# Performance work log

Measured on AMD Instinct MI355X. Metric: run time of the kernel, lower is better.

The kernel has to match this reference:

```python
import jax, jax.numpy as jnp
import numpy as np

D = 768  # feature_dim


def setup_inputs() -> dict:
    key = jax.random.key(0)
    ks = jax.random.split(key, 8)
    B, L = 8, 2048
    vision_features = jax.random.normal(ks[0], (B, L, D), dtype=jnp.float32)
    language_features = jax.random.normal(ks[1], (B, L, D), dtype=jnp.float32)
    s = 1.0 / np.sqrt(D)
    Wv = jax.random.uniform(ks[2], (D, D), jnp.float32, -s, s)
    bv = jax.random.uniform(ks[3], (D,), jnp.float32, -s, s)
    Wl = jax.random.uniform(ks[4], (D, D), jnp.float32, -s, s)
    bl = jax.random.uniform(ks[5], (D,), jnp.float32, -s, s)
    so = 1.0 / np.sqrt(2 * D)
    Wo = jax.random.uniform(ks[6], (D, 2 * D), jnp.float32, -so, so)
    bo = jax.random.uniform(ks[7], (D,), jnp.float32, -so, so)
    return {
        "vision_features": vision_features,
        "language_features": language_features,
        "Wv": Wv, "bv": bv, "Wl": Wl, "bl": bl, "Wo": Wo, "bo": bo,
    }


def reference(vision_features, language_features, Wv, bv, Wl, bl, Wo, bo):
    # linear projections (torch Linear: x @ W^T + b)
    vp = jnp.einsum('bld,ed->ble', vision_features, Wv) + bv      # [B,L,D]
    lp = jnp.einsum('bld,ed->ble', language_features, Wl) + bl    # [B,L,D]
    # unscaled bidirectional attention
    sim = jnp.einsum('bid,bjd->bij', vp, lp)                      # [B,L,L]
    attn = jax.nn.softmax(sim, axis=-1)
    aligned_vision = jnp.einsum('bij,bjd->bid', attn, vp)         # [B,L,D]
    aligned_language = jnp.einsum('bij,bid->bjd', attn, lp)       # attn^T @ lp -> [B,L,D]
    combined = jnp.concatenate([aligned_vision, aligned_language], axis=-1)  # [B,L,2D]
    return jnp.einsum('blc,ec->ble', combined, Wo) + bo           # [B,L,D]
```

## Files before the change

### kernel.cpp

```cpp
#include <hip/hip_runtime.h>
#include <stdint.h>

typedef __attribute__((ext_vector_type(8))) short bf16x8;
typedef __attribute__((ext_vector_type(4))) float f32x4;

__device__ __forceinline__ float b2f(short h) {
  return __uint_as_float(((unsigned)(unsigned short)h) << 16);
}
__device__ __forceinline__ short f2b(float f) {
  unsigned u = __float_as_uint(f);
  u += 0x7fffu + ((u >> 16) & 1u);
  return (short)(u >> 16);
}

__device__ __forceinline__ int swz(int r) { return (r & 6) << 2; }

__device__ __forceinline__ void glds16(const void* g, void* l) {
  __builtin_amdgcn_global_load_lds(
      (const __attribute__((address_space(1))) void*)g,
      (__attribute__((address_space(3))) void*)l, 16, 0, 0);
}

__device__ __forceinline__ void xcd_decode(int C, int RSX, int RPZ,
                                           int& z, int& rowB, int& colB) {
  int id = blockIdx.x;
  int xcd = id & 7, slot = id >> 3;
  int rs = xcd * RSX + slot / C;
  colB = (slot % C) * 128;
  z = rs / RPZ;
  rowB = (rs % RPZ) * 128;
}

__global__ __launch_bounds__(256) void cvt_kernel(
    const float* __restrict__ S0, short* __restrict__ H0, short* __restrict__ L0,
    const float* __restrict__ S1, short* __restrict__ H1, short* __restrict__ L1,
    const float* __restrict__ S2, short* __restrict__ H2, short* __restrict__ L2,
    int n0, int n1, int n2) {
  int g = blockIdx.x * 256 + threadIdx.x;
  const float* s;
  short* h;
  short* l;
  if (g < n0) {
    s = S0 + (size_t)g * 8;
    h = H0 + (size_t)g * 8;
    l = L0 + (size_t)g * 8;
  } else if (g < n0 + n1) {
    size_t t = (size_t)(g - n0);
    s = S1 + t * 8;
    h = H1 + t * 8;
    l = L1 + t * 8;
  } else {
    size_t t = (size_t)(g - n0 - n1);
    s = S2 + t * 8;
    h = H2 + t * 8;
    l = L2 + t * 8;
  }
  float4 v0 = *reinterpret_cast<const float4*>(s);
  float4 v1 = *reinterpret_cast<const float4*>(s + 4);
  float vv[8] = {v0.x, v0.y, v0.z, v0.w, v1.x, v1.y, v1.z, v1.w};
  bf16x8 th, tl;
#pragma unroll
  for (int j = 0; j < 8; ++j) {
    short hh = f2b(vv[j]);
    th[j] = hh;
    tl[j] = f2b(vv[j] - b2f(hh));
  }
  *reinterpret_cast<bf16x8*>(h) = th;
  *reinterpret_cast<bf16x8*>(l) = tl;
}

__global__ __launch_bounds__(256) void rowsum_kernel(const short* __restrict__ P,
                                                     float* __restrict__ invL) {
  int wave = threadIdx.x >> 6, lane = threadIdx.x & 63;
  size_t row = (size_t)blockIdx.x * 4 + wave;
  const short* p = P + row * 2048;
  float s = 0.f;
#pragma unroll
  for (int it = 0; it < 4; ++it) {
    bf16x8 x = *reinterpret_cast<const bf16x8*>(&p[it * 512 + lane * 8]);
#pragma unroll
    for (int j = 0; j < 8; ++j) s += b2f(x[j]);
  }
#pragma unroll
  for (int m = 32; m; m >>= 1) s += __shfl_xor(s, m);
  if (lane == 0) invL[row] = 1.0f / s;
}

__global__ __launch_bounds__(256) void scale_transpose_kernel(
    const short* __restrict__ lp, const float* __restrict__ invL,
    short* __restrict__ lpsT) {
  __shared__ alignas(16) short T[64 * 64];
  int id = blockIdx.x;
  int z = id / 384, r = id % 384;
  int it = r / 12, dt = r % 12;
  int i0 = it * 64, d0 = dt * 64;
  const short* src = lp + (size_t)z * 2048 * 768;
  const float* Lz = invL + (size_t)z * 2048;
  int t = threadIdx.x;
#pragma unroll
  for (int q = 0; q < 2; ++q) {
    int v = t * 2 + q;
    int ii = v >> 3, dc = (v & 7) * 8;
    float s = Lz[i0 + ii];
    bf16x8 x = *reinterpret_cast<const bf16x8*>(&src[(size_t)(i0 + ii) * 768 + d0 + dc]);
    bf16x8 y;
#pragma unroll
    for (int j = 0; j < 8; ++j) y[j] = f2b(b2f(x[j]) * s);
    *reinterpret_cast<bf16x8*>(&T[ii * 64 + (dc ^ ((ii & 7) << 3))]) = y;
  }
  __syncthreads();
  short* dst = lpsT + (size_t)z * 768 * 2048;
#pragma unroll
  for (int q = 0; q < 2; ++q) {
    int v = t * 2 + q;
    int dd = v >> 3, is = (v & 7) * 8;
    bf16x8 y;
#pragma unroll
    for (int s2 = 0; s2 < 8; ++s2) {
      int rr = is + s2;
      y[s2] = T[rr * 64 + (dd ^ ((rr & 7) << 3))];
    }
    *reinterpret_cast<bf16x8*>(&dst[(size_t)(d0 + dd) * 2048 + i0 + is]) = y;
  }
}

__global__ __launch_bounds__(256) void transpose_inplace_kernel(short* __restrict__ P) {
  __shared__ alignas(16) short Ta[64 * 64];
  __shared__ alignas(16) short Tb[64 * 64];
  int id = blockIdx.x;
  int z = id >> 10, r = id & 1023;
  int a = r >> 5, b = r & 31;
  if (a > b) return;
  short* Pz = P + (size_t)z * 2048 * 2048;
  int t = threadIdx.x;
#pragma unroll
  for (int q = 0; q < 2; ++q) {
    int v = t * 2 + q;
    int ii = v >> 3, cc = (v & 7) * 8;
    bf16x8 x = *reinterpret_cast<const bf16x8*>(&Pz[(size_t)(a * 64 + ii) * 2048 + b * 64 + cc]);
    *reinterpret_cast<bf16x8*>(&Ta[ii * 64 + (cc ^ ((ii & 7) << 3))]) = x;
    if (a != b) {
      bf16x8 y = *reinterpret_cast<const bf16x8*>(&Pz[(size_t)(b * 64 + ii) * 2048 + a * 64 + cc]);
      *reinterpret_cast<bf16x8*>(&Tb[ii * 64 + (cc ^ ((ii & 7) << 3))]) = y;
    }
  }
  __syncthreads();
#pragma unroll
  for (int q = 0; q < 2; ++q) {
    int v = t * 2 + q;
    int rr = v >> 3, cs = (v & 7) * 8;
    bf16x8 x, y;
#pragma unroll
    for (int s2 = 0; s2 < 8; ++s2) {
      int rs = cs + s2;
      x[s2] = Ta[rs * 64 + (rr ^ ((rs & 7) << 3))];
      if (a != b) y[s2] = Tb[rs * 64 + (rr ^ ((rs & 7) << 3))];
    }
    *reinterpret_cast<bf16x8*>(&Pz[(size_t)(b * 64 + rr) * 2048 + a * 64 + cs]) = x;
    if (a != b)
      *reinterpret_cast<bf16x8*>(&Pz[(size_t)(a * 64 + rr) * 2048 + b * 64 + cs]) = y;
  }
}

template <bool LO>
__global__ __launch_bounds__(256) void projg_kernel(
    const short* __restrict__ Ah, const short* __restrict__ Al,
    const short* __restrict__ Bh, const short* __restrict__ Bl,
    const float* __restrict__ bias,
    short* __restrict__ Ch, short* __restrict__ Cl) {
  __shared__ alignas(16) short AsH[128 * 32];
  __shared__ alignas(16) short AsL[128 * 32];
  __shared__ alignas(16) short BsH[128 * 32];
  __shared__ alignas(16) short BsL[128 * 32];
  const int tid = threadIdx.x;
  int z, rowBase, colBase;
  xcd_decode(6, 16, 128, z, rowBase, colBase);
  (void)z;
  const int lane = tid & 63;
  const int ln = lane & 15;
  const int qd = lane >> 4;
  const int w = tid >> 6;
  const int wr = w >> 1, wc = w & 1;

  f32x4 acc[4][4];
#pragma unroll
  for (int i = 0; i < 4; ++i)
#pragma unroll
    for (int j = 0; j < 4; ++j) acc[i][j] = 0.f;

  for (int kb = 0; kb < 768; kb += 32) {
#pragma unroll
    for (int q = 0; q < 2; ++q) {
      int c = q * 256 + tid;
      int r = c >> 2;
      int k0 = ((c & 3) << 3) ^ swz(r);
      size_t ao = (size_t)(rowBase + r) * 768 + kb + k0;
      size_t bo = (size_t)(colBase + r) * 768 + kb + k0;
      glds16(&Ah[ao], &AsH[c * 8]);
      glds16(&Al[ao], &AsL[c * 8]);
      glds16(&Bh[bo], &BsH[c * 8]);
      glds16(&Bl[bo], &BsL[c * 8]);
    }
    __syncthreads();
    bf16x8 ah[4], bh[4], t[4];
#pragma unroll
    for (int rt = 0; rt < 4; ++rt) {
      int m = wr * 64 + rt * 16 + ln;
      ah[rt] = *reinterpret_cast<const bf16x8*>(&AsH[m * 32 + ((qd * 8) ^ swz(m))]);
    }
#pragma unroll
    for (int ct = 0; ct < 4; ++ct) {
      int n = wc * 64 + ct * 16 + ln;
      bh[ct] = *reinterpret_cast<const bf16x8*>(&BsH[n * 32 + ((qd * 8) ^ swz(n))]);
    }
#pragma unroll
    for (int rt = 0; rt < 4; ++rt)
#pragma unroll
      for (int ct = 0; ct < 4; ++ct)
        acc[rt][ct] = __builtin_amdgcn_mfma_f32_16x16x32_bf16(ah[rt], bh[ct], acc[rt][ct], 0, 0, 0);
#pragma unroll
    for (int rt = 0; rt < 4; ++rt) {
      int m = wr * 64 + rt * 16 + ln;
      t[rt] = *reinterpret_cast<const bf16x8*>(&AsL[m * 32 + ((qd * 8) ^ swz(m))]);
    }
#pragma unroll
    for (int rt = 0; rt < 4; ++rt)
#pragma unroll
      for (int ct = 0; ct < 4; ++ct)
        acc[rt][ct] = __builtin_amdgcn_mfma_f32_16x16x32_bf16(t[rt], bh[ct], acc[rt][ct], 0, 0, 0);
#pragma unroll
    for (int ct = 0; ct < 4; ++ct) {
      int n = wc * 64 + ct * 16 + ln;
      t[ct] = *reinterpret_cast<const bf16x8*>(&BsL[n * 32 + ((qd * 8) ^ swz(n))]);
    }
#pragma unroll
    for (int rt = 0; rt < 4; ++rt)
#pragma unroll
      for (int ct = 0; ct < 4; ++ct)
        acc[rt][ct] = __builtin_amdgcn_mfma_f32_16x16x32_bf16(ah[rt], t[ct], acc[rt][ct], 0, 0, 0);
    __syncthreads();
  }

#pragma unroll
  for (int rt = 0; rt < 4; ++rt) {
    int row0 = rowBase + wr * 64 + rt * 16 + qd * 4;
#pragma unroll
    for (int ct = 0; ct < 4; ++ct) {
      int col = colBase + wc * 64 + ct * 16 + ln;
      float bb = bias[col];
      f32x4 a = acc[rt][ct];
#pragma unroll
      for (int r = 0; r < 4; ++r) {
        float val = a[r] + bb;
        short h = f2b(val);
        Ch[(size_t)(row0 + r) * 768 + col] = h;
        if constexpr (LO) Cl[(size_t)(row0 + r) * 768 + col] = f2b(val - b2f(h));
      }
    }
  }
}

__global__ __launch_bounds__(256) void sim2_kernel(const short* __restrict__ vp,
                                                   const short* __restrict__ lph,
                                                   const short* __restrict__ lpl,
                                                   short* __restrict__ P) {
  __shared__ alignas(16) short As[128 * 32];
  __shared__ alignas(16) short Bh[128 * 32];
  __shared__ alignas(16) short Bl[128 * 32];
  const int tid = threadIdx.x;
  int z, rowBase, colBase;
  xcd_decode(16, 16, 16, z, rowBase, colBase);
  const short* Az = vp + (size_t)z * 2048 * 768;
  const short* B0 = lph + (size_t)z * 2048 * 768;
  const short* B1 = lpl + (size_t)z * 2048 * 768;
  const int lane = tid & 63;
  const int ln = lane & 15;
  const int qd = lane >> 4;
  const int w = tid >> 6;
  const int wr = w >> 1, wc = w & 1;

  f32x4 acc[4][4];
#pragma unroll
  for (int i = 0; i < 4; ++i)
#pragma unroll
    for (int j = 0; j < 4; ++j) acc[i][j] = 0.f;

  for (int kb = 0; kb < 768; kb += 32) {
#pragma unroll
    for (int q = 0; q < 2; ++q) {
      int c = q * 256 + tid;
      int r = c >> 2;
      int k0 = ((c & 3) << 3) ^ swz(r);
      glds16(&Az[(size_t)(rowBase + r) * 768 + kb + k0], &As[c * 8]);
      glds16(&B0[(size_t)(colBase + r) * 768 + kb + k0], &Bh[c * 8]);
      glds16(&B1[(size_t)(colBase + r) * 768 + kb + k0], &Bl[c * 8]);
    }
    __syncthreads();
    bf16x8 af[4], bf[4];
#pragma unroll
    for (int rt = 0; rt < 4; ++rt) {
      int m = wr * 64 + rt * 16 + ln;
      af[rt] = *reinterpret_cast<const bf16x8*>(&As[m * 32 + ((qd * 8) ^ swz(m))]);
    }
#pragma unroll
    for (int ct = 0; ct < 4; ++ct) {
      int n = wc * 64 + ct * 16 + ln;
      bf[ct] = *reinterpret_cast<const bf16x8*>(&Bh[n * 32 + ((qd * 8) ^ swz(n))]);
    }
#pragma unroll
    for (int rt = 0; rt < 4; ++rt)
#pragma unroll
      for (int ct = 0; ct < 4; ++ct)
        acc[rt][ct] = __builtin_amdgcn_mfma_f32_16x16x32_bf16(af[rt], bf[ct], acc[rt][ct], 0, 0, 0);
#pragma unroll
    for (int ct = 0; ct < 4; ++ct) {
      int n = wc * 64 + ct * 16 + ln;
      bf[ct] = *reinterpret_cast<const bf16x8*>(&Bl[n * 32 + ((qd * 8) ^ swz(n))]);
    }
#pragma unroll
    for (int rt = 0; rt < 4; ++rt)
#pragma unroll
      for (int ct = 0; ct < 4; ++ct)
        acc[rt][ct] = __builtin_amdgcn_mfma_f32_16x16x32_bf16(af[rt], bf[ct], acc[rt][ct], 0, 0, 0);
    __syncthreads();
  }

  short* Pz = P + (size_t)z * 2048 * 2048;
#pragma unroll
  for (int rt = 0; rt < 4; ++rt) {
    int row0 = rowBase + wr * 64 + rt * 16 + qd * 4;
#pragma unroll
    for (int ct = 0; ct < 4; ++ct) {
      int col = colBase + wc * 64 + ct * 16 + ln;
      f32x4 a = acc[rt][ct];
#pragma unroll
      for (int r = 0; r < 4; ++r)
        Pz[(size_t)(row0 + r) * 2048 + col] = f2b(__expf(a[r] - 20.0f));
    }
  }
}

template <int MODE, bool TB, bool SB, bool DUALA>
__global__ __launch_bounds__(256) void gemm_k(const short* __restrict__ A,
                                              const short* __restrict__ A2,
                                              const void* __restrict__ B,
                                              void* __restrict__ C,
                                              const float* __restrict__ bias,
                                              const float* __restrict__ invL,
                                              int C_, int RSX_, int RPZ_,
                                              int K, int ldA, int ldB, int ldC,
                                              long sA, long sB, long sC, long sL) {
  __shared__ alignas(16) short As[128 * 32];
  __shared__ alignas(16) short Bs[128 * 32];
  const int tid = threadIdx.x;
  int z, rowBase, colBase;
  xcd_decode(C_, RSX_, RPZ_, z, rowBase, colBase);
  const short* Az = A + (size_t)z * sA;
  const float* Lz = invL ? (invL + (size_t)z * sL) : nullptr;
  const int lane = tid & 63;
  const int ln = lane & 15;
  const int qd = lane >> 4;
  const int w = tid >> 6;
  const int wr = w >> 1, wc = w & 1;

  f32x4 acc[4][4];
#pragma unroll
  for (int i = 0; i < 4; ++i)
#pragma unroll
    for (int j = 0; j < 4; ++j) acc[i][j] = 0.f;

  for (int kb = 0; kb < K; kb += 32) {
#pragma unroll
    for (int q = 0; q < 2; ++q) {
      int c = q * 256 + tid;
      int r = c >> 2;
      int k0 = ((c & 3) << 3) ^ swz(r);
      int kk = kb + k0;
      const short* src;
      if constexpr (DUALA) {
        src = (kk < 768) ? &Az[(size_t)(rowBase + r) * 768 + kk]
                         : &A2[(size_t)(rowBase + r) * 768 + kk - 768];
      } else {
        src = &Az[(size_t)(rowBase + r) * ldA + kk];
      }
      glds16(src, &As[c * 8]);
    }
    if constexpr (TB) {
      const short* Bz = (const short*)B + (size_t)z * sB;
#pragma unroll
      for (int q = 0; q < 2; ++q) {
        int task = q * 256 + tid;
        int n = task & 127;
        int kc = (task >> 7) << 3;
        bf16x8 t;
#pragma unroll
        for (int s = 0; s < 8; ++s) {
          short v = Bz[(size_t)(kb + kc + s) * ldB + colBase + n];
          if constexpr (SB) v = f2b(b2f(v) * Lz[kb + kc + s]);
          t[s] = v;
        }
        *reinterpret_cast<bf16x8*>(&Bs[n * 32 + (kc ^ swz(n))]) = t;
      }
    } else {
      const short* Bz = (const short*)B + (size_t)z * sB;
#pragma unroll
      for (int q = 0; q < 2; ++q) {
        int c = q * 256 + tid;
        int r = c >> 2;
        int k0 = ((c & 3) << 3) ^ swz(r);
        glds16(&Bz[(size_t)(colBase + r) * ldB + kb + k0], &Bs[c * 8]);
      }
    }
    __syncthreads();
    bf16x8 af[4], bfv[4];
#pragma unroll
    for (int rt = 0; rt < 4; ++rt) {
      int m = wr * 64 + rt * 16 + ln;
      af[rt] = *reinterpret_cast<const bf16x8*>(&As[m * 32 + ((qd * 8) ^ swz(m))]);
    }
#pragma unroll
    for (int ct = 0; ct < 4; ++ct) {
      int n = wc * 64 + ct * 16 + ln;
      bfv[ct] = *reinterpret_cast<const bf16x8*>(&Bs[n * 32 + ((qd * 8) ^ swz(n))]);
    }
#pragma unroll
    for (int rt = 0; rt < 4; ++rt)
#pragma unroll
      for (int ct = 0; ct < 4; ++ct)
        acc[rt][ct] =
            __builtin_amdgcn_mfma_f32_16x16x32_bf16(af[rt], bfv[ct], acc[rt][ct], 0, 0, 0);
    __syncthreads();
  }

#pragma unroll
  for (int rt = 0; rt < 4; ++rt) {
    int row0 = rowBase + wr * 64 + rt * 16 + qd * 4;
#pragma unroll
    for (int ct = 0; ct < 4; ++ct) {
      int col = colBase + wc * 64 + ct * 16 + ln;
      f32x4 a = acc[rt][ct];
      if constexpr (MODE == 2) {
        short* Co = (short*)C + (size_t)z * sC;
#pragma unroll
        for (int r = 0; r < 4; ++r)
          Co[(size_t)(row0 + r) * ldC + col] = f2b(a[r] * Lz[row0 + r]);
      } else if constexpr (MODE == 3) {
        short* Co = (short*)C + (size_t)z * sC;
#pragma unroll
        for (int r = 0; r < 4; ++r) Co[(size_t)(row0 + r) * ldC + col] = f2b(a[r]);
      } else {
        float* Co = (float*)C + (size_t)z * sC;
        float bb = bias[col];
#pragma unroll
        for (int r = 0; r < 4; ++r) Co[(size_t)(row0 + r) * ldC + col] = a[r] + bb;
      }
    }
  }
}

extern "C" void kernel_launch(void* const* d_in, const int* in_sizes, int n_in,
                              void* d_out, int out_size, void* d_ws, size_t ws_size,
                              hipStream_t stream) {
  const float* vf = (const float*)d_in[0];
  const float* lf = (const float*)d_in[1];
  const float* Wv = (const float*)d_in[2];
  const float* bv = (const float*)d_in[3];
  const float* Wl = (const float*)d_in[4];
  const float* bl = (const float*)d_in[5];
  const float* Wo = (const float*)d_in[6];
  const float* bo = (const float*)d_in[7];

  constexpr int Bz = 8, L = 2048, D = 768, M = Bz * L, D2 = 2 * D;
  constexpr size_t PLANE = (size_t)M * D;
  constexpr size_t WPLANE = (size_t)D * D;

  char* wp = (char*)d_ws;
  auto alloc = [&](size_t bytes) {
    char* p = wp;
    wp += (bytes + 255) & ~(size_t)255;
    return p;
  };
  short* vp_hi = (short*)alloc(PLANE * 2);
  short* P     = (short*)alloc((size_t)Bz * L * L * 2);
  float* invL  = (float*)alloc((size_t)M * 4);

  size_t need_direct = (size_t)(wp - (char*)d_ws) + 2 * PLANE * 2 + 512;
  bool direct = ws_size >= need_direct;

  short *lp_hi, *lp_lo;
  if (direct) {
    lp_hi = (short*)alloc(PLANE * 2);
    lp_lo = (short*)alloc(PLANE * 2);
  } else {
    lp_hi = (short*)d_out;
    lp_lo = lp_hi + PLANE;
  }
  short* lpsT = lp_lo;
  short* av   = lp_hi;
  short* al   = vp_hi;
  short* woh = P + 2 * PLANE;
  short* wol = woh + (size_t)D * D2;
  float* out_tmp = direct ? (float*)d_out : (float*)P;

  short* fh  = P;
  short* fl  = P + PLANE;
  short* wvh = P + 2 * PLANE;
  short* wvl = wvh + WPLANE;
  short* wlh = wvl + WPLANE;
  short* wll = wlh + WPLANE;

  constexpr int GF  = (int)(PLANE / 8);
  constexpr int GW  = (int)(WPLANE / 8);
  constexpr int GWO = (int)((size_t)D * D2 / 8);

  cvt_kernel<<<dim3((GF + 2 * GW) / 256), 256, 0, stream>>>(
      vf, fh, fl, Wv, wvh, wvl, Wl, wlh, wll, GF, GW, GW);

  projg_kernel<false><<<dim3(768), 256, 0, stream>>>(fh, fl, wvh, wvl, bv, vp_hi, nullptr);

  cvt_kernel<<<dim3(GF / 256), 256, 0, stream>>>(
      lf, fh, fl, nullptr, nullptr, nullptr, nullptr, nullptr, nullptr, GF, 0, 0);

  projg_kernel<true><<<dim3(768), 256, 0, stream>>>(fh, fl, wlh, wll, bl, lp_hi, lp_lo);

  sim2_kernel<<<dim3(2048), 256, 0, stream>>>(vp_hi, lp_hi, lp_lo, P);

  rowsum_kernel<<<dim3(M / 4), 256, 0, stream>>>(P, invL);

  scale_transpose_kernel<<<dim3(3072), 256, 0, stream>>>(lp_hi, invL, lpsT);

  gemm_k<2, true, false, false><<<dim3(768), 256, 0, stream>>>(
      P, nullptr, vp_hi, av, nullptr, invL, 6, 16, 16, L, L, D, D,
      (long)L * L, (long)L * D, (long)L * D, (long)L);

  transpose_inplace_kernel<<<dim3(8192), 256, 0, stream>>>(P);

  gemm_k<3, false, false, false><<<dim3(768), 256, 0, stream>>>(
      P, nullptr, lpsT, al, nullptr, nullptr, 6, 16, 16, L, L, L, D,
      (long)L * L, (long)D * L, (long)L * D, (long)L);

  cvt_kernel<<<dim3(GWO / 256), 256, 0, stream>>>(
      Wo, woh, wol, nullptr, nullptr, nullptr, nullptr, nullptr, nullptr, GWO, 0, 0);

  gemm_k<4, false, false, true><<<dim3(768), 256, 0, stream>>>(
      av, al, woh, out_tmp, bo, nullptr, 6, 16, 128, D2, D, D2, D, 0, 0, 0, 0);

  if (!direct)
    hipMemcpyAsync(d_out, out_tmp, (size_t)M * D * 4, hipMemcpyDeviceToDevice, stream);
}
```

Before: 657.9 us.

## Use fp16 single-pass MFMA for similarity and fuse row sums via atomics

Result: faster. 643.6 us (-2.2%).

```diff
diff --git a/kernel.cpp b/kernel.cpp
--- a/kernel.cpp
+++ b/kernel.cpp
@@ -2,6 +2,7 @@
 #include <stdint.h>
 
 typedef __attribute__((ext_vector_type(8))) short bf16x8;
+typedef __attribute__((ext_vector_type(8))) _Float16 f16x8;
 typedef __attribute__((ext_vector_type(4))) float f32x4;
 
 __device__ __forceinline__ float b2f(short h) {
@@ -11,6 +12,13 @@
   unsigned u = __float_as_uint(f);
   u += 0x7fffu + ((u >> 16) & 1u);
   return (short)(u >> 16);
+}
+__device__ __forceinline__ short f2h(float f) {
+  _Float16 h = (_Float16)f;
+  return __builtin_bit_cast(short, h);
+}
+__device__ __forceinline__ float h2f(short s) {
+  return (float)__builtin_bit_cast(_Float16, s);
 }
 
 __device__ __forceinline__ int swz(int r) { return (r & 6) << 2; }
@@ -69,21 +77,14 @@
   *reinterpret_cast<bf16x8*>(l) = tl;
 }
 
-__global__ __launch_bounds__(256) void rowsum_kernel(const short* __restrict__ P,
-                                                     float* __restrict__ invL) {
-  int wave = threadIdx.x >> 6, lane = threadIdx.x & 63;
-  size_t row = (size_t)blockIdx.x * 4 + wave;
-  const short* p = P + row * 2048;
-  float s = 0.f;
-#pragma unroll
-  for (int it = 0; it < 4; ++it) {
-    bf16x8 x = *reinterpret_cast<const bf16x8*>(&p[it * 512 + lane * 8]);
-#pragma unroll
-    for (int j = 0; j < 8; ++j) s += b2f(x[j]);
-  }
-#pragma unroll
-  for (int m = 32; m; m >>= 1) s += __shfl_xor(s, m);
-  if (lane == 0) invL[row] = 1.0f / s;
+__global__ __launch_bounds__(256) void zero_kernel(float* __restrict__ p, int n) {
+  int i = blockIdx.x * 256 + threadIdx.x;
+  if (i < n) p[i] = 0.f;
+}
+__global__ __launch_bounds__(256) void recip_kernel(const float* __restrict__ s,
+                                                    float* __restrict__ invL, int n) {
+  int i = blockIdx.x * 256 + threadIdx.x;
+  if (i < n) invL[i] = 1.0f / s[i];
 }
 
 __global__ __launch_bounds__(256) void scale_transpose_kernel(
@@ -162,7 +163,7 @@
   }
 }
 
-template <bool LO>
+template <int OM>
 __global__ __launch_bounds__(256) void projg_kernel(
     const short* __restrict__ Ah, const short* __restrict__ Al,
     const short* __restrict__ Bh, const short* __restrict__ Bl,
@@ -252,27 +253,28 @@
 #pragma unroll
       for (int r = 0; r < 4; ++r) {
         float val = a[r] + bb;
-        short h = f2b(val);
-        Ch[(size_t)(row0 + r) * 768 + col] = h;
-        if constexpr (LO) Cl[(size_t)(row0 + r) * 768 + col] = f2b(val - b2f(h));
+        if constexpr (OM == 0) {
+          Ch[(size_t)(row0 + r) * 768 + col] = f2h(val);
+        } else {
+          Ch[(size_t)(row0 + r) * 768 + col] = f2b(val);
+          Cl[(size_t)(row0 + r) * 768 + col] = f2h(val);
+        }
       }
     }
   }
 }
 
 __global__ __launch_bounds__(256) void sim2_kernel(const short* __restrict__ vp,
-                                                   const short* __restrict__ lph,
-                                                   const short* __restrict__ lpl,
-                                                   short* __restrict__ P) {
+                                                   const short* __restrict__ lp,
+                                                   short* __restrict__ P,
+                                                   float* __restrict__ S) {
   __shared__ alignas(16) short As[128 * 32];
-  __shared__ alignas(16) short Bh[128 * 32];
-  __shared__ alignas(16) short Bl[128 * 32];
+  __shared__ alignas(16) short Bs[128 * 32];
   const int tid = threadIdx.x;
   int z, rowBase, colBase;
   xcd_decode(16, 16, 16, z, rowBase, colBase);
   const short* Az = vp + (size_t)z * 2048 * 768;
-  const short* B0 = lph + (size_t)z * 2048 * 768;
-  const short* B1 = lpl + (size_t)z * 2048 * 768;
+  const short* Bz = lp + (size_t)z * 2048 * 768;
   const int lane = tid & 63;
   const int ln = lane & 15;
   const int qd = lane >> 4;
@@ -292,55 +294,58 @@
       int r = c >> 2;
       int k0 = ((c & 3) << 3) ^ swz(r);
       glds16(&Az[(size_t)(rowBase + r) * 768 + kb + k0], &As[c * 8]);
-      glds16(&B0[(size_t)(colBase + r) * 768 + kb + k0], &Bh[c * 8]);
-      glds16(&B1[(size_t)(colBase + r) * 768 + kb + k0], &Bl[c * 8]);
+      glds16(&Bz[(size_t)(colBase + r) * 768 + kb + k0], &Bs[c * 8]);
     }
     __syncthreads();
-    bf16x8 af[4], bf[4];
+    f16x8 af[4], bf[4];
 #pragma unroll
     for (int rt = 0; rt < 4; ++rt) {
       int m = wr * 64 + rt * 16 + ln;
-      af[rt] = *reinterpret_cast<const bf16x8*>(&As[m * 32 + ((qd * 8) ^ swz(m))]);
+      af[rt] = *reinterpret_cast<const f16x8*>(&As[m * 32 + ((qd * 8) ^ swz(m))]);
     }
 #pragma unroll
     for (int ct = 0; ct < 4; ++ct) {
       int n = wc * 64 + ct * 16 + ln;
-      bf[ct] = *reinterpret_cast<const bf16x8*>(&Bh[n * 32 + ((qd * 8) ^ swz(n))]);
+      bf[ct] = *reinterpret_cast<const f16x8*>(&Bs[n * 32 + ((qd * 8) ^ swz(n))]);
     }
 #pragma unroll
     for (int rt = 0; rt < 4; ++rt)
 #pragma unroll
       for (int ct = 0; ct < 4; ++ct)
-        acc[rt][ct] = __builtin_amdgcn_mfma_f32_16x16x32_bf16(af[rt], bf[ct], acc[rt][ct], 0, 0, 0);
-#pragma unroll
-    for (int ct = 0; ct < 4; ++ct) {
-      int n = wc * 64 + ct * 16 + ln;
-      bf[ct] = *reinterpret_cast<const bf16x8*>(&Bl[n * 32 + ((qd * 8) ^ swz(n))]);
-    }
-#pragma unroll
-    for (int rt = 0; rt < 4; ++rt)
-#pragma unroll
-      for (int ct = 0; ct < 4; ++ct)
-        acc[rt][ct] = __builtin_amdgcn_mfma_f32_16x16x32_bf16(af[rt], bf[ct], acc[rt][ct], 0, 0, 0);
+        acc[rt][ct] = __builtin_amdgcn_mfma_f32_16x16x32_f16(af[rt], bf[ct], acc[rt][ct], 0, 0, 0);
     __syncthreads();
   }
 
   short* Pz = P + (size_t)z * 2048 * 2048;
+  float* Sz = S + (size_t)z * 2048;
 #pragma unroll
   for (int rt = 0; rt < 4; ++rt) {
     int row0 = rowBase + wr * 64 + rt * 16 + qd * 4;
+    float rowp[4] = {0.f, 0.f, 0.f, 0.f};
 #pragma unroll
     for (int ct = 0; ct < 4; ++ct) {
       int col = colBase + wc * 64 + ct * 16 + ln;
       f32x4 a = acc[rt][ct];
 #pragma unroll
-      for (int r = 0; r < 4; ++r)
-        Pz[(size_t)(row0 + r) * 2048 + col] = f2b(__expf(a[r] - 20.0f));
-    }
-  }
-}
-
-template <int MODE, bool TB, bool SB, bool DUALA>
+      for (int r = 0; r < 4; ++r) {
+        short h = f2b(__expf(a[r] - 20.0f));
+        Pz[(size_t)(row0 + r) * 2048 + col] = h;
+        rowp[r] += b2f(h);
+      }
+    }
+#pragma unroll
+    for (int r = 0; r < 4; ++r) {
+      float v = rowp[r];
+      v += __shfl_xor(v, 1);
+      v += __shfl_xor(v, 2);
+      v += __shfl_xor(v, 4);
+      v += __shfl_xor(v, 8);
+      if (ln == 0) atomicAdd(&Sz[row0 + r], v);
+    }
+  }
+}
+
+template <int MODE, bool TB, bool SB, bool F16B, bool DUALA>
 __global__ __launch_bounds__(256) void gemm_k(const short* __restrict__ A,
                                               const short* __restrict__ A2,
                                               const void* __restrict__ B,
@@ -396,6 +401,7 @@
 #pragma unroll
         for (int s = 0; s < 8; ++s) {
           short v = Bz[(size_t)(kb + kc + s) * ldB + colBase + n];
+          if constexpr (F16B) v = f2b(h2f(v));
           if constexpr (SB) v = f2b(b2f(v) * Lz[kb + kc + s]);
           t[s] = v;
         }
@@ -480,24 +486,25 @@
     wp += (bytes + 255) & ~(size_t)255;
     return p;
   };
-  short* vp_hi = (short*)alloc(PLANE * 2);
+  short* vp16  = (short*)alloc(PLANE * 2);
   short* P     = (short*)alloc((size_t)Bz * L * L * 2);
   float* invL  = (float*)alloc((size_t)M * 4);
+  float* sums  = (float*)alloc((size_t)M * 4);
 
   size_t need_direct = (size_t)(wp - (char*)d_ws) + 2 * PLANE * 2 + 512;
   bool direct = ws_size >= need_direct;
 
-  short *lp_hi, *lp_lo;
+  short *lp_bf, *lp16;
   if (direct) {
-    lp_hi = (short*)alloc(PLANE * 2);
-    lp_lo = (short*)alloc(PLANE * 2);
+    lp_bf = (short*)alloc(PLANE * 2);
+    lp16  = (short*)alloc(PLANE * 2);
   } else {
-    lp_hi = (short*)d_out;
-    lp_lo = lp_hi + PLANE;
-  }
-  short* lpsT = lp_lo;
-  short* av   = lp_hi;
-  short* al   = vp_hi;
+    lp_bf = (short*)d_out;
+    lp16  = lp_bf + PLANE;
+  }
+  short* lpsT = lp16;
+  short* av   = lp_bf;
+  short* al   = vp16;
   short* woh = P + 2 * PLANE;
   short* wol = woh + (size_t)D * D2;
   float* out_tmp = direct ? (float*)d_out : (float*)P;
@@ -513,36 +520,38 @@
   constexpr int GW  = (int)(WPLANE / 8);
   constexpr int GWO = (int)((size_t)D * D2 / 8);
 
+  zero_kernel<<<dim3(M / 256), 256, 0, stream>>>(sums, M);
+
   cvt_kernel<<<dim3((GF + 2 * GW) / 256), 256, 0, stream>>>(
       vf, fh, fl, Wv, wvh, wvl, Wl, wlh, wll, GF, GW, GW);
 
-  projg_kernel<false><<<dim3(768), 256, 0, stream>>>(fh, fl, wvh, wvl, bv, vp_hi, nullptr);
+  projg_kernel<0><<<dim3(768), 256, 0, stream>>>(fh, fl, wvh, wvl, bv, vp16, nullptr);
 
   cvt_kernel<<<dim3(GF / 256), 256, 0, stream>>>(
       lf, fh, fl, nullptr, nullptr, nullptr, nullptr, nullptr, nullptr, GF, 0, 0);
 
-  projg_kernel<true><<<dim3(768), 256, 0, stream>>>(fh, fl, wlh, wll, bl, lp_hi, lp_lo);
-
-  sim2_kernel<<<dim3(2048), 256, 0, stream>>>(vp_hi, lp_hi, lp_lo, P);
-
-  rowsum_kernel<<<dim3(M / 4), 256, 0, stream>>>(P, invL);
-
-  scale_transpose_kernel<<<dim3(3072), 256, 0, stream>>>(lp_hi, invL, lpsT);
-
-  gemm_k<2, true, false, false><<<dim3(768), 256, 0, stream>>>(
-      P, nullptr, vp_hi, av, nullptr, invL, 6, 16, 16, L, L, D, D,
+  projg_kernel<1><<<dim3(768), 256, 0, stream>>>(fh, fl, wlh, wll, bl, lp_bf, lp16);
+
+  sim2_kernel<<<dim3(2048), 256, 0, stream>>>(vp16, lp16, P, sums);
+
+  recip_kernel<<<dim3(M / 256), 256, 0, stream>>>(sums, invL, M);
+
+  scale_transpose_kernel<<<dim3(3072), 256, 0, stream>>>(lp_bf, invL, lpsT);
+
+  gemm_k<2, true, false, true, false><<<dim3(768), 256, 0, stream>>>(
+      P, nullptr, vp16, av, nullptr, invL, 6, 16, 16, L, L, D, D,
       (long)L * L, (long)L * D, (long)L * D, (long)L);
 
   transpose_inplace_kernel<<<dim3(8192), 256, 0, stream>>>(P);
 
-  gemm_k<3, false, false, false><<<dim3(768), 256, 0, stream>>>(
+  gemm_k<3, false, false, false, false><<<dim3(768), 256, 0, stream>>>(
       P, nullptr, lpsT, al, nullptr, nullptr, 6, 16, 16, L, L, L, D,
       (long)L * L, (long)D * L, (long)L * D, (long)L);
 
   cvt_kernel<<<dim3(GWO / 256), 256, 0, stream>>>(
       Wo, woh, wol, nullptr, nullptr, nullptr, nullptr, nullptr, nullptr, GWO, 0, 0);
 
-  gemm_k<4, false, false, true><<<dim3(768), 256, 0, stream>>>(
+  gemm_k<4, false, false, false, true><<<dim3(768), 256, 0, stream>>>(
       av, al, woh, out_tmp, bo, nullptr, 6, 16, 128, D2, D, D2, D, 0, 0, 0, 0);
 
   if (!direct)
```
